# Kernel optimization log

Measured on AMD Instinct MI355X. Metric: run time of the kernel, lower is better.

Reference implementation:

```python
import jax, jax.numpy as jnp
import numpy as np

Kk = 4; B = 32768; Nn = 10; F_IN = 3; F_H = 16; F_OUT = 8; HOPS = 3


def _tagconv(x, row, col, norm, W, b, n):
    # TAGConv: out = sum_k A_norm^k x W_k + b  (W: [HOPS+1, in, out])
    out = x @ W[0]
    h = x
    for k in range(1, W.shape[0]):
        h = jax.ops.segment_sum(h[row] * norm[:, None], col, num_segments=n)
        out = out + h @ W[k]
    return out + b


def setup_inputs() -> dict:
    key = jax.random.key(0)
    ks = jax.random.split(key, 8)
    G = Kk * B
    totN = G * Nn
    E1 = Nn * (Nn - 1)
    # fully-connected (no self loop) edge pattern per 10-node graph, offset per graph
    i = jnp.repeat(jnp.arange(Nn), Nn); j = jnp.tile(jnp.arange(Nn), Nn)
    m = i != j
    sl = i[m]; dl = j[m]                      # [90]
    off = (jnp.arange(G) * Nn)[:, None]
    edge_index = jnp.stack([(off + sl[None, :]).reshape(-1),
                            (off + dl[None, :]).reshape(-1)], 0)
    x = jax.random.normal(ks[0], (totN, F_IN), jnp.float32)
    edge_weight = jax.random.uniform(ks[1], (G * E1,), jnp.float32)
    eigen = jax.random.uniform(ks[2], (G,), jnp.float32)
    a_0 = jnp.ones((1,), jnp.float32)
    W0 = jax.random.normal(ks[3], (HOPS + 1, F_IN, F_H), jnp.float32) / np.sqrt(F_IN)
    b0 = jnp.zeros((F_H,), jnp.float32)
    W1 = jax.random.normal(ks[4], (HOPS + 1, F_H, F_OUT), jnp.float32) / np.sqrt(F_H)
    b1 = jnp.zeros((F_OUT,), jnp.float32)
    bp_w = jax.random.normal(ks[5], (F_OUT,), jnp.float32) / np.sqrt(F_OUT)
    cp_w = jax.random.normal(ks[6], (F_OUT,), jnp.float32) / np.sqrt(F_OUT)
    w_w = jax.random.normal(ks[7], (F_OUT, F_OUT), jnp.float32) / np.sqrt(F_OUT)
    return {"x": x, "edge_index": edge_index, "edge_weight": edge_weight,
            "K": Kk, "batch_size": B, "N": Nn, "eigen": eigen, "a_0": a_0,
            "W0": W0, "b0": b0, "W1": W1, "b1": b1,
            "bp_w": bp_w, "cp_w": cp_w, "w_w": w_w}


def reference(x, edge_index, edge_weight, K, batch_size, N, eigen, a_0,
              W0, b0, W1, b1, bp_w, cp_w, w_w):
    totN = x.shape[0]
    G = K * batch_size
    E1 = N * (N - 1)
    row, col = edge_index[0], edge_index[1]
    # --- vectorized replacement of the K*batch loop over to_dense_adj ---
    w_kbe = edge_weight.reshape(K, batch_size, E1)
    src = edge_index[0, :E1]
    dst = edge_index[1, :E1]
    R = jnp.zeros((K, batch_size, N, N), x.dtype).at[:, :, src, dst].add(w_kbe)
    R = R * eigen.reshape(K, batch_size)[:, :, None, None]
    # --- GCN symmetric norm (no self loops), as in PyG TAGConv ---
    deg = jax.ops.segment_sum(edge_weight, col, num_segments=totN)
    dinv = jnp.where(deg > 0, deg ** -0.5, 0.0).astype(x.dtype)
    norm = dinv[row] * edge_weight * dinv[col]
    y = jax.nn.leaky_relu(_tagconv(x, row, col, norm, W0, b0, totN))
    y = jax.nn.leaky_relu(_tagconv(y, row, col, norm, W1, b1, totN))
    a_y = y @ bp_w            # [totN]
    t_y = y @ cp_w            # [totN]
    yw = (y @ w_w.T).reshape(G, N, -1)
    yb = y.reshape(G, N, -1)
    K_y = jnp.einsum('gnd,gmd->gnm', yw, yb).reshape(K, batch_size, N, N)
    k_ij = jax.nn.softmax(K_y, axis=0)   # softmax over the K states axis
    path_mod = jnp.maximum(x[:, 2], 0.0).reshape(G, N)
    a_ik = (a_0[0] + jax.nn.relu(a_y)).reshape(K, batch_size, N)
    t_k = t_y.reshape(G, N) * (1.0 - path_mod)
    t_k = jnp.where(t_k == 0.0, jnp.asarray(-1e10, t_k.dtype), t_k)
    t_j = jax.nn.softmax(t_k.reshape(K, batch_size, N), axis=0)
    R_t = jnp.swapaxes(R, 2, 3)
    return (k_ij, a_ik, t_j, R, R_t)
```

## Files before the change

kernel.cpp:

```cpp
#include <hip/hip_runtime.h>

#define KK 4
#define BATCH 32768
#define NN 10
#define GPW 6
#define SLAB 132
#define NTHREADS 256

static constexpr size_t OFF_AIK = (size_t)KK * BATCH * NN * NN;
static constexpr size_t OFF_TJ  = OFF_AIK + (size_t)KK * BATCH * NN;
static constexpr size_t OFF_R   = OFF_TJ  + (size_t)KK * BATCH * NN;
static constexpr size_t OFF_RT  = OFF_R   + (size_t)KK * BATCH * NN * NN;

#define WSYNC() do { asm volatile("" ::: "memory"); \
                     __builtin_amdgcn_wave_barrier(); \
                     asm volatile("" ::: "memory"); } while (0)

__device__ __forceinline__ float rcpf(float x) {
#if __has_builtin(__builtin_amdgcn_rcpf)
    return __builtin_amdgcn_rcpf(x);
#else
    return 1.f / x;
#endif
}
__device__ __forceinline__ float fexp2(float x) {
#if __has_builtin(__builtin_amdgcn_exp2f)
    return __builtin_amdgcn_exp2f(x);
#else
    return exp2f(x);
#endif
}

static __device__ __forceinline__ float2 pk_mul2(float2 a, float2 b) {
    float2 d; asm("v_pk_mul_f32 %0, %1, %2" : "=v"(d) : "v"(a), "v"(b)); return d; }
static __device__ __forceinline__ float2 pk_add2(float2 a, float2 b) {
    float2 d; asm("v_pk_add_f32 %0, %1, %2" : "=v"(d) : "v"(a), "v"(b)); return d; }
static __device__ __forceinline__ float2 pk_fma2(float2 a, float2 b, float2 c) {
    float2 d; asm("v_pk_fma_f32 %0, %1, %2, %3" : "=v"(d) : "v"(a), "v"(b), "v"(c)); return d; }
static __device__ __forceinline__ float2 pk_fma_blo(float2 a, float2 b, float2 c) {
    float2 d; asm("v_pk_fma_f32 %0, %1, %2, %3 op_sel_hi:[0,1,1]"
                  : "=v"(d) : "v"(a), "v"(b), "v"(c)); return d; }
static __device__ __forceinline__ float2 pk_fma_bhi(float2 a, float2 b, float2 c) {
    float2 d; asm("v_pk_fma_f32 %0, %1, %2, %3 op_sel:[1,0,0] op_sel_hi:[1,1,1]"
                  : "=v"(d) : "v"(a), "v"(b), "v"(c)); return d; }
static __device__ __forceinline__ float2 pk_fma_blo_s(float2 a, float2 bs, float2 c) {
    float2 d; asm("v_pk_fma_f32 %0, %1, %2, %3 op_sel_hi:[0,1,1]"
                  : "=v"(d) : "v"(a), "s"(bs), "v"(c)); return d; }
static __device__ __forceinline__ float2 pk_fma_bhi_s(float2 a, float2 bs, float2 c) {
    float2 d; asm("v_pk_fma_f32 %0, %1, %2, %3 op_sel:[1,0,0] op_sel_hi:[1,1,1]"
                  : "=v"(d) : "v"(a), "s"(bs), "v"(c)); return d; }
static __device__ __forceinline__ float2 pk_mul_blo_s(float2 a, float2 bs) {
    float2 d; asm("v_pk_mul_f32 %0, %1, %2 op_sel_hi:[0,1]"
                  : "=v"(d) : "v"(a), "s"(bs)); return d; }
static __device__ __forceinline__ float2 pk_fma_vs(float2 a, float2 bs, float2 c) {
    float2 d; asm("v_pk_fma_f32 %0, %1, %2, %3" : "=v"(d) : "v"(a), "s"(bs), "v"(c)); return d; }
static __device__ __forceinline__ float2 pk_add_vs(float2 a, float2 bs) {
    float2 d; asm("v_pk_add_f32 %0, %1, %2" : "=v"(d) : "v"(a), "s"(bs)); return d; }
static __device__ __forceinline__ float2 el_max2(float2 a, float2 b) {
    return make_float2(fmaxf(a.x, b.x), fmaxf(a.y, b.y)); }
static __device__ __forceinline__ float2 leaky2(float2 v) {
    return make_float2(fmaxf(v.x, 0.f) + 0.01f * fminf(v.x, 0.f),
                       fmaxf(v.y, 0.f) + 0.01f * fminf(v.y, 0.f)); }

__global__ __launch_bounds__(NTHREADS, 8)
void gnn_fused(const float* __restrict__ xin,
               const float* __restrict__ ew,
               const float* __restrict__ eigen,
               const float* __restrict__ a0p,
               const float* __restrict__ W0p,
               const float* __restrict__ b0p,
               const float* __restrict__ W1p,
               const float* __restrict__ b1p,
               const float* __restrict__ bpp,
               const float* __restrict__ cpp,
               const float* __restrict__ wwp,
               float* __restrict__ out)
{
    __shared__ __align__(16) float sm[KK * GPW * SLAB];

    const float LOG2E = 1.4426950408889634f;

    const int t = threadIdx.x;
    const int l = t & 63;
    const int w = t >> 6;
    int s = l / 10;
    const int n = l % 10;
    const bool dup = (s >= GPW);
    if (dup) s = GPW - 1;
    const int bb0 = blockIdx.x * GPW;
    const int bb  = bb0 + s;
    const bool valid = (!dup) && (bb < BATCH);
    const int bbc = (bb < BATCH) ? bb : (BATCH - 1);
    const int g   = w * BATCH + bbc;

    float* slab = sm + (w * GPW + s) * SLAB;

    {
        const int nvb = min(GPW, BATCH - bb0);
        const float* ewK = ew + ((size_t)w * BATCH + bb0) * 90;
        float* wbase = sm + w * GPW * SLAB;
        const unsigned lim = (unsigned)(nvb * 45);
#pragma unroll
        for (int it = 0; it < 5; ++it) {
            unsigned i2 = (unsigned)(it * 64 + l);
            if (i2 < lim) {
                float2 v = *(const float2*)(ewK + (size_t)i2 * 2);
                unsigned sg = i2 / 45u, off = i2 - sg * 45u;
                *(float2*)(wbase + sg * SLAB + off * 2) = v;
            }
        }
    }

    const size_t node = (size_t)g * NN + n;
    const float x0 = xin[node * 3 + 0];
    const float x1 = xin[node * 3 + 1];
    const float x2 = xin[node * 3 + 2];
    const float eig = eigen[g];
    const float a0v = a0p[0];

    WSYNC();

    float rowv[9];
    {
        const float* rp = slab + n * 9;
#pragma unroll
        for (int c = 0; c < 9; ++c) rowv[c] = rp[c];
    }
    float wout[10];
    wout[0] = (n == 0) ? 0.f : rowv[0];
    wout[9] = (n == 9) ? 0.f : rowv[8];
#pragma unroll
    for (int j = 1; j < 9; ++j)
        wout[j] = (j == n) ? 0.f : ((j < n) ? rowv[j] : rowv[j - 1]);

    WSYNC();
#pragma unroll
    for (int j = 0; j < 10; ++j) slab[j * 10 + n] = wout[j];
    WSYNC();
    float2 win2[5];
    {
        const float* rp = slab + n * 10;
#pragma unroll
        for (int q = 0; q < 5; ++q) win2[q] = *(const float2*)(rp + 2 * q);
    }
    const float deg = (win2[0].x + win2[0].y) + (win2[1].x + win2[1].y)
                    + (win2[2].x + win2[2].y) + (win2[3].x + win2[3].y)
                    + (win2[4].x + win2[4].y);

    if (valid) {
        float* pr = out + OFF_R  + (size_t)g * 100 + n * 10;
        float* pt = out + OFF_RT + (size_t)g * 100 + n * 10;
#pragma unroll
        for (int q = 0; q < 5; ++q) {
            ((float2*)pr)[q] = make_float2(wout[2*q] * eig, wout[2*q+1] * eig);
            ((float2*)pt)[q] = make_float2(win2[q].x * eig, win2[q].y * eig);
        }
    }

    const float dv = (deg > 0.f) ? __frsqrt_rn(deg) : 0.f;
    slab[120 + n] = dv;
    WSYNC();
    float2 dinv2[5];
#pragma unroll
    for (int q = 0; q < 5; ++q) dinv2[q] = *(const float2*)(slab + 120 + 2 * q);
    const float2 dv2 = make_float2(dv, dv);
    float2 arow2[5];
#pragma unroll
    for (int q = 0; q < 5; ++q)
        arow2[q] = pk_mul2(pk_mul2(dinv2[q], win2[q]), dv2);

    const float2 x01 = make_float2(x0, x1);
    const float2 x2p = make_float2(x2, 0.f);
    float2 acc0p[8];
#pragma unroll
    for (int q = 0; q < 8; ++q) {
        float2 wa = *(const float2*)(W0p + 2*q);
        float2 wb = *(const float2*)(W0p + 16 + 2*q);
        float2 wc = *(const float2*)(W0p + 32 + 2*q);
        acc0p[q] = pk_mul_blo_s(x01, wa);
        acc0p[q] = pk_fma_bhi_s(x01, wb, acc0p[q]);
        acc0p[q] = pk_fma_blo_s(x2p, wc, acc0p[q]);
    }
    {
        float2 hab = x01, hcj = x2p;
#pragma unroll
        for (int hop = 1; hop <= 3; ++hop) {
            *(float2*)(slab + n * 12)     = hab;
            *(float2*)(slab + n * 12 + 2) = hcj;
            WSYNC();
            float2 nab = make_float2(0.f, 0.f), ncj = make_float2(0.f, 0.f);
#pragma unroll
            for (int m = 0; m < 10; ++m) {
                const float4 hm = *(const float4*)(slab + m * 12);
                const float2 hx = make_float2(hm.x, hm.y);
                const float2 hz = make_float2(hm.z, hm.w);
                const float2 am = arow2[m >> 1];
                if ((m & 1) == 0) {
                    nab = pk_fma_blo(am, hx, nab);
                    ncj = pk_fma_blo(am, hz, ncj);
                } else {
                    nab = pk_fma_bhi(am, hx, nab);
                    ncj = pk_fma_bhi(am, hz, ncj);
                }
            }
            WSYNC();
#pragma unroll
            for (int q = 0; q < 8; ++q) {
                float2 wa = *(const float2*)(W0p + hop*48 + 2*q);
                float2 wb = *(const float2*)(W0p + hop*48 + 16 + 2*q);
                float2 wc = *(const float2*)(W0p + hop*48 + 32 + 2*q);
                acc0p[q] = pk_fma_blo_s(nab, wa, acc0p[q]);
                acc0p[q] = pk_fma_bhi_s(nab, wb, acc0p[q]);
                acc0p[q] = pk_fma_blo_s(ncj, wc, acc0p[q]);
            }
            hab = nab; hcj = ncj;
        }
    }
    const float2 zero2 = make_float2(0.f, 0.f);
    float2 y1p[8];
#pragma unroll
    for (int q = 0; q < 8; ++q) {
        float2 b2 = *(const float2*)(b0p + 2*q);
        y1p[q] = leaky2(pk_add_vs(acc0p[q], b2));
    }

    float2 cur2[4];
#pragma unroll
    for (int q = 0; q < 4; ++q) {
        float2 w0 = *(const float2*)(W1p + 384 + 2*q);
        cur2[q] = pk_mul_blo_s(y1p[0], w0);
        float2 w1 = *(const float2*)(W1p + 384 + 8 + 2*q);
        cur2[q] = pk_fma_bhi_s(y1p[0], w1, cur2[q]);
#pragma unroll
        for (int p8 = 1; p8 < 8; ++p8) {
            float2 wl = *(const float2*)(W1p + 384 + (2*p8)*8 + 2*q);
            float2 wh = *(const float2*)(W1p + 384 + (2*p8+1)*8 + 2*q);
            cur2[q] = pk_fma_blo_s(y1p[p8], wl, cur2[q]);
            cur2[q] = pk_fma_bhi_s(y1p[p8], wh, cur2[q]);
        }
    }
#pragma unroll
    for (int kh = 2; kh >= 0; --kh) {
        *(float2*)(slab + n * 12)     = cur2[0];
        *(float2*)(slab + n * 12 + 2) = cur2[1];
        *(float2*)(slab + n * 12 + 4) = cur2[2];
        *(float2*)(slab + n * 12 + 6) = cur2[3];
        WSYNC();
        float2 ag[4] = {zero2, zero2, zero2, zero2};
#pragma unroll
        for (int m = 0; m < 10; ++m) {
            const float4 p = *(const float4*)(slab + m * 12);
            const float4 r = *(const float4*)(slab + m * 12 + 4);
            const float2 pa = make_float2(p.x, p.y), pb = make_float2(p.z, p.w);
            const float2 ra = make_float2(r.x, r.y), rb = make_float2(r.z, r.w);
            const float2 am = arow2[m >> 1];
            if ((m & 1) == 0) {
                ag[0] = pk_fma_blo(am, pa, ag[0]);
                ag[1] = pk_fma_blo(am, pb, ag[1]);
                ag[2] = pk_fma_blo(am, ra, ag[2]);
                ag[3] = pk_fma_blo(am, rb, ag[3]);
            } else {
                ag[0] = pk_fma_bhi(am, pa, ag[0]);
                ag[1] = pk_fma_bhi(am, pb, ag[1]);
                ag[2] = pk_fma_bhi(am, ra, ag[2]);
                ag[3] = pk_fma_bhi(am, rb, ag[3]);
            }
        }
        WSYNC();
#pragma unroll
        for (int q = 0; q < 4; ++q) {
            cur2[q] = ag[q];
#pragma unroll
            for (int p8 = 0; p8 < 8; ++p8) {
                float2 wl = *(const float2*)(W1p + kh*128 + (2*p8)*8 + 2*q);
                float2 wh = *(const float2*)(W1p + kh*128 + (2*p8+1)*8 + 2*q);
                cur2[q] = pk_fma_blo_s(y1p[p8], wl, cur2[q]);
                cur2[q] = pk_fma_bhi_s(y1p[p8], wh, cur2[q]);
            }
        }
    }
    float2 y2p[4];
#pragma unroll
    for (int q = 0; q < 4; ++q) {
        float2 b2 = *(const float2*)(b1p + 2*q);
        y2p[q] = leaky2(pk_add_vs(cur2[q], b2));
    }

    *(float2*)(slab + n * 12)     = y2p[0];
    *(float2*)(slab + n * 12 + 2) = y2p[1];
    *(float2*)(slab + n * 12 + 4) = y2p[2];
    *(float2*)(slab + n * 12 + 6) = y2p[3];

    float2 accA = zero2, accT = zero2;
#pragma unroll
    for (int q = 0; q < 4; ++q) {
        float2 bp2 = *(const float2*)(bpp + 2*q);
        float2 cp2 = *(const float2*)(cpp + 2*q);
        accA = pk_fma_vs(y2p[q], bp2, accA);
        accT = pk_fma_vs(y2p[q], cp2, accT);
    }
    const float ay = accA.x + accA.y;
    const float ty = accT.x + accT.y;
    if (valid)
        out[OFF_AIK + (size_t)g * 10 + n] = a0v + fmaxf(ay, 0.f);

    float tk = ty * (1.f - fmaxf(x2, 0.f));
    if (tk == 0.f) tk = -1e10f;
    const float tks = tk * LOG2E;

    float2 yw2[4];
#pragma unroll
    for (int qd = 0; qd < 4; ++qd) {
        float2 aA = zero2, aB = zero2;
#pragma unroll
        for (int q = 0; q < 4; ++q) {
            float2 wA = *(const float2*)(wwp + (2*qd)*8 + 2*q);
            float2 wB = *(const float2*)(wwp + (2*qd+1)*8 + 2*q);
            aA = pk_fma_vs(y2p[q], wA, aA);
            aB = pk_fma_vs(y2p[q], wB, aB);
        }
        yw2[qd] = make_float2(aA.x + aA.y, aB.x + aB.y);
    }
    WSYNC();
    float kyr[10];
#pragma unroll
    for (int m = 0; m < 10; ++m) {
        const float4 p = *(const float4*)(slab + m * 12);
        const float4 r = *(const float4*)(slab + m * 12 + 4);
        float2 acc = pk_mul2(yw2[0], make_float2(p.x, p.y));
        acc = pk_fma2(yw2[1], make_float2(p.z, p.w), acc);
        acc = pk_fma2(yw2[2], make_float2(r.x, r.y), acc);
        acc = pk_fma2(yw2[3], make_float2(r.z, r.w), acc);
        kyr[m] = (acc.x + acc.y) * LOG2E;
    }
    WSYNC();
#pragma unroll
    for (int q = 0; q < 5; ++q)
        *(float2*)(slab + n * 12 + 2*q) = make_float2(kyr[2*q], kyr[2*q+1]);
    slab[120 + n] = tks;

    __syncthreads();

    {
        const float tv0 = sm[(0*GPW + s)*SLAB + 120 + n];
        const float tv1 = sm[(1*GPW + s)*SLAB + 120 + n];
        const float tv2 = sm[(2*GPW + s)*SLAB + 120 + n];
        const float tv3 = sm[(3*GPW + s)*SLAB + 120 + n];
        const float mx = fmaxf(fmaxf(tv0, tv1), fmaxf(tv2, tv3));
        const float den = fexp2(tv0-mx) + fexp2(tv1-mx) + fexp2(tv2-mx) + fexp2(tv3-mx);
        if (valid)
            out[OFF_TJ + (size_t)g * 10 + n] = fexp2(tks - mx) * rcpf(den);
    }
    {
        const float* k0 = sm + (0*GPW + s)*SLAB + n * 12;
        const float* k1 = sm + (1*GPW + s)*SLAB + n * 12;
        const float* k2 = sm + (2*GPW + s)*SLAB + n * 12;
        const float* k3 = sm + (3*GPW + s)*SLAB + n * 12;
        float* po = out + (size_t)g * 100 + n * 10;
#pragma unroll
        for (int q = 0; q < 5; ++q) {
            const float2 a = *(const float2*)(k0 + 2*q);
            const float2 b = *(const float2*)(k1 + 2*q);
            const float2 c = *(const float2*)(k2 + 2*q);
            const float2 d = *(const float2*)(k3 + 2*q);
            const float2 mx2v = el_max2(el_max2(a, b), el_max2(c, d));
            const float dl = fexp2(a.x-mx2v.x) + fexp2(b.x-mx2v.x)
                           + fexp2(c.x-mx2v.x) + fexp2(d.x-mx2v.x);
            const float dh = fexp2(a.y-mx2v.y) + fexp2(b.y-mx2v.y)
                           + fexp2(c.y-mx2v.y) + fexp2(d.y-mx2v.y);
            const float2 own = *(const float2*)(slab + n * 12 + 2*q);
            if (valid)
                ((float2*)po)[q] = make_float2(fexp2(own.x - mx2v.x) * rcpf(dl),
                                               fexp2(own.y - mx2v.y) * rcpf(dh));
        }
    }
}

extern "C" void kernel_launch(void* const* d_in, const int* in_sizes, int n_in,
                              void* d_out, int out_size, void* d_ws, size_t ws_size,
                              hipStream_t stream) {
    const float* x   = (const float*)d_in[0];
    const float* ew  = (const float*)d_in[2];
    const float* eig = (const float*)d_in[6];
    const float* a0  = (const float*)d_in[7];
    const float* W0  = (const float*)d_in[8];
    const float* b0  = (const float*)d_in[9];
    const float* W1  = (const float*)d_in[10];
    const float* b1  = (const float*)d_in[11];
    const float* bpw = (const float*)d_in[12];
    const float* cpw = (const float*)d_in[13];
    const float* www = (const float*)d_in[14];
    float* out = (float*)d_out;

    const int grid = (BATCH + GPW - 1) / GPW;
    gnn_fused<<<dim3(grid), dim3(NTHREADS), 0, stream>>>(
        x, ew, eig, a0, W0, b0, W1, b1, bpw, cpw, www, out);
}
```

Measured before the change: 77.69 us.

## Load edge weights directly per thread, widen LDS stores, reuse softmax exponentials

The coalesced cooperative staging of edge weights into LDS is dropped; each thread now reads its own 9 edge weights straight from global memory, which removes one LDS round trip and one wave barrier. The R output store moves earlier, right after the row is built, and paired float2 LDS stores become float4 stores. The final softmaxes reuse the already-computed exponential for the thread's own state through a select instead of recomputing it, and the K_y slab uses a stride of 10. The trade-off is that the per-thread global reads of 9 floats at stride 9 are less coalesced than the old staged loads.

```diff
diff --git a/kernel.cpp b/kernel.cpp
--- a/kernel.cpp
+++ b/kernel.cpp
@@ -33,8 +33,6 @@
 
 static __device__ __forceinline__ float2 pk_mul2(float2 a, float2 b) {
     float2 d; asm("v_pk_mul_f32 %0, %1, %2" : "=v"(d) : "v"(a), "v"(b)); return d; }
-static __device__ __forceinline__ float2 pk_add2(float2 a, float2 b) {
-    float2 d; asm("v_pk_add_f32 %0, %1, %2" : "=v"(d) : "v"(a), "v"(b)); return d; }
 static __device__ __forceinline__ float2 pk_fma2(float2 a, float2 b, float2 c) {
     float2 d; asm("v_pk_fma_f32 %0, %1, %2, %3" : "=v"(d) : "v"(a), "v"(b), "v"(c)); return d; }
 static __device__ __forceinline__ float2 pk_fma_blo(float2 a, float2 b, float2 c) {
@@ -87,30 +85,19 @@
     const int n = l % 10;
     const bool dup = (s >= GPW);
     if (dup) s = GPW - 1;
-    const int bb0 = blockIdx.x * GPW;
-    const int bb  = bb0 + s;
+    const int bb  = blockIdx.x * GPW + s;
     const bool valid = (!dup) && (bb < BATCH);
     const int bbc = (bb < BATCH) ? bb : (BATCH - 1);
     const int g   = w * BATCH + bbc;
 
     float* slab = sm + (w * GPW + s) * SLAB;
 
-    {
-        const int nvb = min(GPW, BATCH - bb0);
-        const float* ewK = ew + ((size_t)w * BATCH + bb0) * 90;
-        float* wbase = sm + w * GPW * SLAB;
-        const unsigned lim = (unsigned)(nvb * 45);
-#pragma unroll
-        for (int it = 0; it < 5; ++it) {
-            unsigned i2 = (unsigned)(it * 64 + l);
-            if (i2 < lim) {
-                float2 v = *(const float2*)(ewK + (size_t)i2 * 2);
-                unsigned sg = i2 / 45u, off = i2 - sg * 45u;
-                *(float2*)(wbase + sg * SLAB + off * 2) = v;
-            }
-        }
-    }
-
+    float rowv[9];
+    {
+        const float* rp = ew + (size_t)g * 90 + n * 9;
+#pragma unroll
+        for (int c = 0; c < 9; ++c) rowv[c] = rp[c];
+    }
     const size_t node = (size_t)g * NN + n;
     const float x0 = xin[node * 3 + 0];
     const float x1 = xin[node * 3 + 1];
@@ -118,14 +105,6 @@
     const float eig = eigen[g];
     const float a0v = a0p[0];
 
-    WSYNC();
-
-    float rowv[9];
-    {
-        const float* rp = slab + n * 9;
-#pragma unroll
-        for (int c = 0; c < 9; ++c) rowv[c] = rp[c];
-    }
     float wout[10];
     wout[0] = (n == 0) ? 0.f : rowv[0];
     wout[9] = (n == 9) ? 0.f : rowv[8];
@@ -133,7 +112,13 @@
     for (int j = 1; j < 9; ++j)
         wout[j] = (j == n) ? 0.f : ((j < n) ? rowv[j] : rowv[j - 1]);
 
-    WSYNC();
+    if (valid) {
+        float* pr = out + OFF_R + (size_t)g * 100 + n * 10;
+#pragma unroll
+        for (int q = 0; q < 5; ++q)
+            ((float2*)pr)[q] = make_float2(wout[2*q] * eig, wout[2*q+1] * eig);
+    }
+
 #pragma unroll
     for (int j = 0; j < 10; ++j) slab[j * 10 + n] = wout[j];
     WSYNC();
@@ -148,13 +133,10 @@
                     + (win2[4].x + win2[4].y);
 
     if (valid) {
-        float* pr = out + OFF_R  + (size_t)g * 100 + n * 10;
         float* pt = out + OFF_RT + (size_t)g * 100 + n * 10;
 #pragma unroll
-        for (int q = 0; q < 5; ++q) {
-            ((float2*)pr)[q] = make_float2(wout[2*q] * eig, wout[2*q+1] * eig);
+        for (int q = 0; q < 5; ++q)
             ((float2*)pt)[q] = make_float2(win2[q].x * eig, win2[q].y * eig);
-        }
     }
 
     const float dv = (deg > 0.f) ? __frsqrt_rn(deg) : 0.f;
@@ -185,8 +167,7 @@
         float2 hab = x01, hcj = x2p;
 #pragma unroll
         for (int hop = 1; hop <= 3; ++hop) {
-            *(float2*)(slab + n * 12)     = hab;
-            *(float2*)(slab + n * 12 + 2) = hcj;
+            *(float4*)(slab + n * 12) = make_float4(hab.x, hab.y, hcj.x, hcj.y);
             WSYNC();
             float2 nab = make_float2(0.f, 0.f), ncj = make_float2(0.f, 0.f);
 #pragma unroll
@@ -241,10 +222,8 @@
     }
 #pragma unroll
     for (int kh = 2; kh >= 0; --kh) {
-        *(float2*)(slab + n * 12)     = cur2[0];
-        *(float2*)(slab + n * 12 + 2) = cur2[1];
-        *(float2*)(slab + n * 12 + 4) = cur2[2];
-        *(float2*)(slab + n * 12 + 6) = cur2[3];
+        *(float4*)(slab + n * 12)     = make_float4(cur2[0].x, cur2[0].y, cur2[1].x, cur2[1].y);
+        *(float4*)(slab + n * 12 + 4) = make_float4(cur2[2].x, cur2[2].y, cur2[3].x, cur2[3].y);
         WSYNC();
         float2 ag[4] = {zero2, zero2, zero2, zero2};
 #pragma unroll
@@ -286,10 +265,8 @@
         y2p[q] = leaky2(pk_add_vs(cur2[q], b2));
     }
 
-    *(float2*)(slab + n * 12)     = y2p[0];
-    *(float2*)(slab + n * 12 + 2) = y2p[1];
-    *(float2*)(slab + n * 12 + 4) = y2p[2];
-    *(float2*)(slab + n * 12 + 6) = y2p[3];
+    *(float4*)(slab + n * 12)     = make_float4(y2p[0].x, y2p[0].y, y2p[1].x, y2p[1].y);
+    *(float4*)(slab + n * 12 + 4) = make_float4(y2p[2].x, y2p[2].y, y2p[3].x, y2p[3].y);
 
     float2 accA = zero2, accT = zero2;
 #pragma unroll
@@ -336,7 +313,7 @@
     WSYNC();
 #pragma unroll
     for (int q = 0; q < 5; ++q)
-        *(float2*)(slab + n * 12 + 2*q) = make_float2(kyr[2*q], kyr[2*q+1]);
+        *(float2*)(slab + n * 10 + 2*q) = make_float2(kyr[2*q], kyr[2*q+1]);
     slab[120 + n] = tks;
 
     __syncthreads();
@@ -347,15 +324,18 @@
         const float tv2 = sm[(2*GPW + s)*SLAB + 120 + n];
         const float tv3 = sm[(3*GPW + s)*SLAB + 120 + n];
         const float mx = fmaxf(fmaxf(tv0, tv1), fmaxf(tv2, tv3));
-        const float den = fexp2(tv0-mx) + fexp2(tv1-mx) + fexp2(tv2-mx) + fexp2(tv3-mx);
+        const float e0 = fexp2(tv0-mx), e1 = fexp2(tv1-mx);
+        const float e2 = fexp2(tv2-mx), e3 = fexp2(tv3-mx);
+        const float den = e0 + e1 + e2 + e3;
+        const float own = (w == 0) ? e0 : (w == 1) ? e1 : (w == 2) ? e2 : e3;
         if (valid)
-            out[OFF_TJ + (size_t)g * 10 + n] = fexp2(tks - mx) * rcpf(den);
-    }
-    {
-        const float* k0 = sm + (0*GPW + s)*SLAB + n * 12;
-        const float* k1 = sm + (1*GPW + s)*SLAB + n * 12;
-        const float* k2 = sm + (2*GPW + s)*SLAB + n * 12;
-        const float* k3 = sm + (3*GPW + s)*SLAB + n * 12;
+            out[OFF_TJ + (size_t)g * 10 + n] = own * rcpf(den);
+    }
+    {
+        const float* k0 = sm + (0*GPW + s)*SLAB + n * 10;
+        const float* k1 = sm + (1*GPW + s)*SLAB + n * 10;
+        const float* k2 = sm + (2*GPW + s)*SLAB + n * 10;
+        const float* k3 = sm + (3*GPW + s)*SLAB + n * 10;
         float* po = out + (size_t)g * 100 + n * 10;
 #pragma unroll
         for (int q = 0; q < 5; ++q) {
@@ -364,14 +344,16 @@
             const float2 c = *(const float2*)(k2 + 2*q);
             const float2 d = *(const float2*)(k3 + 2*q);
             const float2 mx2v = el_max2(el_max2(a, b), el_max2(c, d));
-            const float dl = fexp2(a.x-mx2v.x) + fexp2(b.x-mx2v.x)
-                           + fexp2(c.x-mx2v.x) + fexp2(d.x-mx2v.x);
-            const float dh = fexp2(a.y-mx2v.y) + fexp2(b.y-mx2v.y)
-                           + fexp2(c.y-mx2v.y) + fexp2(d.y-mx2v.y);
-            const float2 own = *(const float2*)(slab + n * 12 + 2*q);
+            const float eax = fexp2(a.x-mx2v.x), ebx = fexp2(b.x-mx2v.x);
+            const float ecx = fexp2(c.x-mx2v.x), edx = fexp2(d.x-mx2v.x);
+            const float eay = fexp2(a.y-mx2v.y), eby = fexp2(b.y-mx2v.y);
+            const float ecy = fexp2(c.y-mx2v.y), edy = fexp2(d.y-mx2v.y);
+            const float dl = eax + ebx + ecx + edx;
+            const float dh = eay + eby + ecy + edy;
+            const float ox = (w == 0) ? eax : (w == 1) ? ebx : (w == 2) ? ecx : edx;
+            const float oy = (w == 0) ? eay : (w == 1) ? eby : (w == 2) ? ecy : edy;
             if (valid)
-                ((float2*)po)[q] = make_float2(fexp2(own.x - mx2v.x) * rcpf(dl),
-                                               fexp2(own.y - mx2v.y) * rcpf(dh));
+                ((float2*)po)[q] = make_float2(ox * rcpf(dl), oy * rcpf(dh));
         }
     }
 }
```

Result: faster. 75.97 us (-2.2%).
